# Kernel tuning notes

Hardware: AMD Instinct MI355X
Metric: run time of the kernel (lower is better)

## Reference

```python
import jax, jax.numpy as jnp
import numpy as np

N = 20000      # num_nodes
E = 256000     # num_edges (before self loops)
D_IN = 128
HID = 128      # hidden_dim (per-head out channels)
HEADS = 4
T = 2          # num_timesteps
NEG_SLOPE = 0.2
LN_EPS = 1e-5


def setup_inputs() -> dict:
    key = jax.random.key(0)
    ks = jax.random.split(key, 24)
    def rn(k, shape, s=0.05):
        return jax.random.normal(k, shape, jnp.float32) * s
    HH = HEADS * HID  # 512
    return {
        "x": jax.random.normal(ks[0], (N, D_IN), jnp.float32),
        "edge_index": jax.random.randint(ks[1], (2, E), 0, N),
        # input projection
        "Wp": rn(ks[2], (HID, D_IN)), "bp": jnp.zeros((HID,), jnp.float32),
        # GAT layer 0: in=HID, heads=HEADS, concat
        "W0": rn(ks[3], (HH, HID)), "as0": rn(ks[4], (HEADS, HID)), "ad0": rn(ks[5], (HEADS, HID)), "b0": jnp.zeros((HH,), jnp.float32),
        # GAT layer 1: in=HH, heads=HEADS, concat
        "W1": rn(ks[6], (HH, HH)), "as1": rn(ks[7], (HEADS, HID)), "ad1": rn(ks[8], (HEADS, HID)), "b1": jnp.zeros((HH,), jnp.float32),
        # GAT layer 2 (last): in=HH, heads=1, concat=False
        "W2": rn(ks[9], (HID, HH)), "as2": rn(ks[10], (1, HID)), "ad2": rn(ks[11], (1, HID)), "b2": jnp.zeros((HID,), jnp.float32),
        # layer norms (dims 512, 512, 128)
        "g0": jnp.ones((HH,), jnp.float32), "be0": jnp.zeros((HH,), jnp.float32),
        "g1": jnp.ones((HH,), jnp.float32), "be1": jnp.zeros((HH,), jnp.float32),
        "g2": jnp.ones((HID,), jnp.float32), "be2": jnp.zeros((HID,), jnp.float32),
        # temporal MultiheadAttention (embed=HID, 4 heads)
        "Wqkv": rn(ks[12], (3 * HID, HID)), "bqkv": jnp.zeros((3 * HID,), jnp.float32),
        "Wo": rn(ks[13], (HID, HID)), "bo": jnp.zeros((HID,), jnp.float32),
    }


def _layernorm(x, g, b):
    mu = x.mean(-1, keepdims=True)
    var = ((x - mu) ** 2).mean(-1, keepdims=True)
    return (x - mu) * jax.lax.rsqrt(var + LN_EPS) * g + b


def _gat_conv(h, src, dst, W, a_src, a_dst, bias, heads, concat):
    # h: [N, in]; W: [heads*HID, in]; a_src/a_dst: [heads, HID]
    xp = (h @ W.T).reshape(N, heads, HID)            # [N, heads, HID]
    al_s = (xp * a_src).sum(-1)                      # [N, heads]
    al_d = (xp * a_dst).sum(-1)                      # [N, heads]
    e = jax.nn.leaky_relu(al_s[src] + al_d[dst], NEG_SLOPE)  # [Etot, heads]
    m = jax.ops.segment_max(e, dst, num_segments=N)          # segment softmax over dst
    e = jnp.exp(e - m[dst])
    s = jax.ops.segment_sum(e, dst, num_segments=N)
    alpha = e / (s[dst] + 1e-16)                     # [Etot, heads]
    msg = xp[src] * alpha[:, :, None]                # [Etot, heads, HID]
    out = jax.ops.segment_sum(msg, dst, num_segments=N)      # [N, heads, HID]
    out = out.reshape(N, heads * HID) if concat else out.mean(1)
    return out + bias


def _forward(x, edge_index, Wp, bp, W0, as0, ad0, b0, W1, as1, ad1, b1,
             W2, as2, ad2, b2, g0, be0, g1, be1, g2, be2, Wqkv, bqkv, Wo, bo):
    loops = jnp.arange(N, dtype=edge_index.dtype)    # add_self_loops=True
    src = jnp.concatenate([edge_index[0], loops])
    dst = jnp.concatenate([edge_index[1], loops])

    h = x @ Wp.T + bp                                 # [N, HID]
    layers = [
        (W0, as0, ad0, b0, HEADS, True, g0, be0),
        (W1, as1, ad1, b1, HEADS, True, g1, be1),
        (W2, as2, ad2, b2, 1, False, g2, be2),
    ]
    states = []
    for t in range(T):
        h_t = h
        for i, (W, a_s, a_d, b, heads, concat, g, be) in enumerate(layers):
            h_res = h_t
            h_t = _gat_conv(h_t, src, dst, W, a_s, a_d, b, heads, concat)
            h_t = jax.nn.elu(h_t)
            h_t = _layernorm(h_t, g, be)
            # dropout is identity in eval mode
            if i > 0:
                if h_res.shape[-1] != h_t.shape[-1]:
                    # adaptive_avg_pool1d 512 -> 128: mean over groups of 4
                    r = h_res.shape[-1] // h_t.shape[-1]
                    h_res = h_res.reshape(N, h_t.shape[-1], r).mean(-1)
                h_t = h_t + h_res
        states.append(h_t)
        h = h_t

    ts = jnp.stack(states, axis=1)                    # [N, T, HID]
    # temporal self-attention (4 heads, head_dim = HID//4)
    nh, hd = 4, HID // 4
    qkv = ts @ Wqkv.T + bqkv                          # [N, T, 3*HID]
    q, k, v = jnp.split(qkv, 3, axis=-1)
    q = q.reshape(N, T, nh, hd).transpose(0, 2, 1, 3)
    k = k.reshape(N, T, nh, hd).transpose(0, 2, 1, 3)
    v = v.reshape(N, T, nh, hd).transpose(0, 2, 1, 3)
    attn = jax.nn.softmax(jnp.einsum("nhqd,nhkd->nhqk", q, k) / jnp.sqrt(jnp.float32(hd)), axis=-1)
    o = jnp.einsum("nhqk,nhkd->nhqd", attn, v).transpose(0, 2, 1, 3).reshape(N, T, HID)
    o = o @ Wo.T + bo
    return o.mean(axis=1)                             # [N, HID]


def reference(x, edge_index, Wp, bp, W0, as0, ad0, b0, W1, as1, ad1, b1,
              W2, as2, ad2, b2, g0, be0, g1, be1, g2, be2, Wqkv, bqkv, Wo, bo):
    return _forward(x, edge_index, Wp, bp, W0, as0, ad0, b0, W1, as1, ad1, b1,
                    W2, as2, ad2, b2, g0, be0, g1, be1, g2, be2, Wqkv, bqkv, Wo, bo)
```

## Files before the change

kernel.cpp:

```cpp
#include <hip/hip_runtime.h>
#include <math.h>

#define N_NODES 20000
#define N_EDGES 256000
#define ETOT (N_EDGES + N_NODES)
#define NPAD 20096
#define NPAD2 40064
#define NBLK_SCAN ((N_NODES + 255) / 256)

typedef __attribute__((ext_vector_type(8))) short bf16x8;
typedef __attribute__((ext_vector_type(4))) float f32x4;

__device__ __forceinline__ unsigned short f2bf(float f) {
    unsigned int u = __builtin_bit_cast(unsigned int, f);
    u = (u + 0x7fff + ((u >> 16) & 1)) >> 16;
    return (unsigned short)u;
}

__device__ __forceinline__ float bf2f(unsigned short u) {
    return __builtin_bit_cast(float, (unsigned int)u << 16);
}

__device__ __forceinline__ void gload_lds16(const void* g, void* l) {
    __builtin_amdgcn_global_load_lds(
        (const __attribute__((address_space(1))) void*)g,
        (__attribute__((address_space(3))) void*)l, 16, 0, 0);
}

__device__ __forceinline__ void fma8(float* acc, uint4 v, float w) {
    acc[0] = fmaf(w, __builtin_bit_cast(float, v.x << 16), acc[0]);
    acc[1] = fmaf(w, __builtin_bit_cast(float, v.x & 0xffff0000u), acc[1]);
    acc[2] = fmaf(w, __builtin_bit_cast(float, v.y << 16), acc[2]);
    acc[3] = fmaf(w, __builtin_bit_cast(float, v.y & 0xffff0000u), acc[3]);
    acc[4] = fmaf(w, __builtin_bit_cast(float, v.z << 16), acc[4]);
    acc[5] = fmaf(w, __builtin_bit_cast(float, v.z & 0xffff0000u), acc[5]);
    acc[6] = fmaf(w, __builtin_bit_cast(float, v.w << 16), acc[6]);
    acc[7] = fmaf(w, __builtin_bit_cast(float, v.w & 0xffff0000u), acc[7]);
}


__global__ void hist_kernel(const int* __restrict__ ei, int* __restrict__ cnt) {
    for (int e = blockIdx.x * blockDim.x + threadIdx.x; e < ETOT;
         e += gridDim.x * blockDim.x) {
        int d = (e < N_EDGES) ? ei[N_EDGES + e] : (e - N_EDGES);
        atomicAdd(&cnt[d], 1);
    }
}

__global__ __launch_bounds__(256) void scanA(const int* __restrict__ cnt,
                                             int* __restrict__ incl,
                                             int* __restrict__ bsum) {
    __shared__ int sh[256];
    int t = threadIdx.x;
    int i = blockIdx.x * 256 + t;
    int v = (i < N_NODES) ? cnt[i] : 0;
    sh[t] = v;
    __syncthreads();
#pragma unroll
    for (int off = 1; off < 256; off <<= 1) {
        int u = (t >= off) ? sh[t - off] : 0;
        __syncthreads();
        sh[t] += u;
        __syncthreads();
    }
    if (i < N_NODES) incl[i] = sh[t];
    if (t == 255) bsum[blockIdx.x] = sh[255];
}

__global__ __launch_bounds__(128) void scanB(int* __restrict__ bsum,
                                             int* __restrict__ row_start) {
    __shared__ int sh[128];
    int t = threadIdx.x;
    int v = (t < NBLK_SCAN) ? bsum[t] : 0;
    sh[t] = v;
    __syncthreads();
#pragma unroll
    for (int off = 1; off < 128; off <<= 1) {
        int u = (t >= off) ? sh[t - off] : 0;
        __syncthreads();
        sh[t] += u;
        __syncthreads();
    }
    if (t < NBLK_SCAN) bsum[t] = sh[t] - v;
    if (t == 0) row_start[0] = 0;
}

__global__ __launch_bounds__(256) void scanC(int* __restrict__ cursor,
                                             int* __restrict__ row_start,
                                             const int* __restrict__ bsum) {
    int i = blockIdx.x * 256 + threadIdx.x;
    if (i < N_NODES) {
        int incl = row_start[i + 1] + bsum[blockIdx.x];
        row_start[i + 1] = incl;
        cursor[i] = incl - cursor[i];
    }
}

__global__ void scatter_kernel(const int* __restrict__ ei, int* __restrict__ cursor,
                               int* __restrict__ sorted_id) {
    for (int e = blockIdx.x * blockDim.x + threadIdx.x; e < ETOT;
         e += gridDim.x * blockDim.x) {
        int d = (e < N_EDGES) ? ei[N_EDGES + e] : (e - N_EDGES);
        int pos = atomicAdd(&cursor[d], 1);
        sorted_id[pos] = e;
    }
}

__global__ __launch_bounds__(256) void segsort_kernel(
    const int* __restrict__ ei, const int* __restrict__ row_start,
    int* __restrict__ sorted_id, int* __restrict__ sorted_src) {
    int wv = threadIdx.x >> 6, lane = threadIdx.x & 63;
    int n = blockIdx.x * 4 + wv;
    if (n >= N_NODES) return;
    int base = row_start[n];
    int deg = row_start[n + 1] - base;
    if (deg <= 64) {
        int id = (lane < deg) ? sorted_id[base + lane] : 0x7fffffff;
        int rank = 0;
        for (int j = 0; j < deg; j++) {
            int idj = __shfl(id, j);
            rank += (idj < id);
        }
        if (lane < deg) {
            int src = (id < N_EDGES) ? ei[id] : (id - N_EDGES);
            sorted_src[base + rank] = src;
        }
    } else if (lane == 0) {
        for (int i = base + 1; i < base + deg; i++) {
            int v = sorted_id[i];
            int j = i - 1;
            while (j >= base && sorted_id[j] > v) {
                sorted_id[j + 1] = sorted_id[j];
                j--;
            }
            sorted_id[j + 1] = v;
        }
        for (int i = base; i < base + deg; i++) {
            int id = sorted_id[i];
            sorted_src[i] = (id < N_EDGES) ? ei[id] : (id - N_EDGES);
        }
    }
}

struct SetupArgs {
    const float* s[7];
    unsigned short* d[7];
    int cum[8];
    int* cursor;
    unsigned short* x16;
    unsigned short* h16n;
    unsigned short* h16wA;
    unsigned short* h16wB;
    unsigned short* st16;
    unsigned short* om16;
};

__global__ __launch_bounds__(256) void setup_all(SetupArgs a) {
    int i = blockIdx.x * 256 + threadIdx.x;
    const int PR = NPAD - N_NODES;
    if (i < N_NODES) a.cursor[i] = 0;
    if (i < PR * 128) {
        a.x16[(size_t)N_NODES * 128 + i] = 0;
        a.h16n[(size_t)N_NODES * 128 + i] = 0;
        a.om16[(size_t)N_NODES * 128 + i] = 0;
    }
    if (i < PR * 512) {
        a.h16wA[(size_t)N_NODES * 512 + i] = 0;
        a.h16wB[(size_t)N_NODES * 512 + i] = 0;
    }
    if (i < (NPAD2 - 2 * N_NODES) * 128) a.st16[(size_t)(2 * N_NODES) * 128 + i] = 0;
    if (i < a.cum[7]) {
        int r = 0;
        while (i >= a.cum[r + 1]) r++;
        int off = i - a.cum[r];
        a.d[r][off] = f2bf(a.s[r][off]);
    }
}

__global__ __launch_bounds__(256) void gemm_mfma(
    const unsigned short* __restrict__ A, const unsigned short* __restrict__ B,
    const float* __restrict__ bias, float* __restrict__ Cf,
    unsigned short* __restrict__ C16, int R, int K, int ldc,
    const float* __restrict__ a_s, const float* __restrict__ a_d,
    float* __restrict__ al_s, float* __restrict__ al_d, int H) {
    __shared__ unsigned short Al[64 * 64];
    __shared__ unsigned short Bl[128 * 64];
    __shared__ float red_s[4][32], red_d[4][32];
    int tid = threadIdx.x;
    int lane = tid & 63, wv = tid >> 6;
    int wr = (wv >> 1) * 32, wc = (wv & 1) * 64;
    size_t br = (size_t)blockIdx.x * 64;
    size_t bc = (size_t)blockIdx.y * 128;
    f32x4 acc[2][4] = {};
    for (int k0 = 0; k0 < K; k0 += 64) {
#pragma unroll
        for (int i = 0; i < 2; i++) {
            int idx = i * 256 + tid;
            int row = idx >> 3;
            int kb = (idx & 7) << 4;
            gload_lds16((const char*)(A + (br + row) * K + k0) + kb,
                        (char*)Al + idx * 16);
        }
#pragma unroll
        for (int i = 0; i < 4; i++) {
            int idx = i * 256 + tid;
            int row = idx >> 3;
            int kb = (idx & 7) << 4;
            gload_lds16((const char*)(B + (bc + row) * K + k0) + kb,
                        (char*)Bl + idx * 16);
        }
        __syncthreads();
#pragma unroll
        for (int kk = 0; kk < 2; kk++) {
            bf16x8 af[2], bfr[4];
#pragma unroll
            for (int m = 0; m < 2; m++)
                af[m] = *(const bf16x8*)&Al[(wr + m * 16 + (lane & 15)) * 64 +
                                            kk * 32 + (lane >> 4) * 8];
#pragma unroll
            for (int n = 0; n < 4; n++)
                bfr[n] = *(const bf16x8*)&Bl[(wc + n * 16 + (lane & 15)) * 64 +
                                             kk * 32 + (lane >> 4) * 8];
#pragma unroll
            for (int m = 0; m < 2; m++)
#pragma unroll
                for (int n = 0; n < 4; n++)
                    acc[m][n] = __builtin_amdgcn_mfma_f32_16x16x32_bf16(
                        af[m], bfr[n], acc[m][n], 0, 0, 0);
        }
        __syncthreads();
    }

    if (al_s) {
        float asr[4], adr[4];
#pragma unroll
        for (int n = 0; n < 4; n++) {
            int c = (int)bc + wc + n * 16 + (lane & 15);
            asr[n] = a_s[c];
            adr[n] = a_d[c];
        }
        float ps[2][4], pd[2][4];
#pragma unroll
        for (int m = 0; m < 2; m++)
#pragma unroll
            for (int j = 0; j < 4; j++) {
                float s = 0.f, d = 0.f;
#pragma unroll
                for (int n = 0; n < 4; n++) {
                    float v = acc[m][n][j];
                    s = fmaf(v, asr[n], s);
                    d = fmaf(v, adr[n], d);
                }
#pragma unroll
                for (int off = 8; off; off >>= 1) {
                    s += __shfl_xor(s, off);
                    d += __shfl_xor(d, off);
                }
                ps[m][j] = s;
                pd[m][j] = d;
            }
        if ((lane & 15) == 0) {
#pragma unroll
            for (int m = 0; m < 2; m++)
#pragma unroll
                for (int j = 0; j < 4; j++) {
                    int lr = m * 16 + (lane >> 4) * 4 + j;
                    red_s[wv][lr] = ps[m][j];
                    red_d[wv][lr] = pd[m][j];
                }
        }
        __syncthreads();
        if (tid < 64) {
            int half = tid >> 5, lr = tid & 31;
            float s = red_s[half * 2][lr] + red_s[half * 2 + 1][lr];
            float d = red_d[half * 2][lr] + red_d[half * 2 + 1][lr];
            size_t r = br + half * 32 + lr;
            if (r < (size_t)R) {
                al_s[r * H + blockIdx.y] = s;
                al_d[r * H + blockIdx.y] = d;
            }
        }
    }

#pragma unroll
    for (int m = 0; m < 2; m++) {
        int r0 = wr + m * 16 + (lane >> 4) * 4;
#pragma unroll
        for (int n = 0; n < 4; n++) {
            int c = (int)bc + wc + n * 16 + (lane & 15);
            float bv = bias ? bias[c] : 0.f;
#pragma unroll
            for (int j = 0; j < 4; j++) {
                size_t r = br + r0 + j;
                if (r < (size_t)R) {
                    float v = acc[m][n][j] + bv;
                    if (Cf) Cf[r * ldc + c] = v;
                    if (C16) C16[r * ldc + c] = f2bf(v);
                }
            }
        }
    }
}

template <int RES>
__global__ __launch_bounds__(256) void gat_agg512(
    const unsigned short* __restrict__ xp16, const float* __restrict__ al_s,
    const float* __restrict__ al_d, const int* __restrict__ row_start,
    const int* __restrict__ srcs, const float* __restrict__ bias,
    const float* __restrict__ gamma, const float* __restrict__ beta,
    const unsigned short* __restrict__ h_res16, unsigned short* __restrict__ out16) {
    const int C = 512;
    int tid = threadIdx.x;
    int lane = tid & 63, wv = tid >> 6;
    int n = blockIdx.x * 4 + wv;
    __shared__ int offw[4][64];
    __shared__ float logw[4][256];
    if (n >= N_NODES) return;
    int base = row_start[n];
    int deg = row_start[n + 1] - base;
    int head = lane >> 4;

    float acc[8] = {};
    float scale_end;

    if (deg <= 64) {
        int e_ = lane >> 2, h_ = lane & 3;
        float m = -3.4e38f;
        for (int e0 = 0; e0 < deg; e0 += 16) {
            int e = e0 + e_;
            float v = -3.4e38f;
            if (e < deg) {
                int src = srcs[base + e];
                if (h_ == 0) offw[wv][e] = src * (C * 2);
                float t = al_s[src * 4 + h_] + al_d[n * 4 + h_];
                v = t > 0.f ? t : 0.2f * t;
                logw[wv][e * 4 + h_] = v;
            }
            m = fmaxf(m, v);
        }
#pragma unroll
        for (int off = 4; off <= 32; off <<= 1) m = fmaxf(m, __shfl_xor(m, off));
        float s = 0.f;
        for (int e0 = 0; e0 < deg; e0 += 16) {
            int e = e0 + e_;
            if (e < deg) {
                float p = __expf(logw[wv][e * 4 + h_] - m);
                logw[wv][e * 4 + h_] = p;
                s += p;
            }
        }
#pragma unroll
        for (int off = 4; off <= 32; off <<= 1) s += __shfl_xor(s, off);
        float inv = 1.0f / (s + 1e-16f);
        scale_end = __shfl(inv, head);
        const char* xb = (const char*)xp16 + lane * 16;
#pragma unroll 4
        for (int j = 0; j < deg; j++) {
            float w = logw[wv][j * 4 + head];
            uint4 vv = *(const uint4*)(xb + offw[wv][j]);
            fma8(acc, vv, w);
        }
    } else {
        int e_ = lane >> 2, h_ = lane & 3;
        float m = -3.4e38f;
        for (int e0 = 0; e0 < deg; e0 += 16) {
            int e = e0 + e_;
            if (e < deg) {
                int src = srcs[base + e];
                float t = al_s[src * 4 + h_] + al_d[n * 4 + h_];
                t = t > 0.f ? t : 0.2f * t;
                m = fmaxf(m, t);
            }
        }
#pragma unroll
        for (int off = 4; off <= 32; off <<= 1) m = fmaxf(m, __shfl_xor(m, off));
        float s = 0.f;
        for (int e0 = 0; e0 < deg; e0 += 16) {
            int e = e0 + e_;
            if (e < deg) {
                int src = srcs[base + e];
                float t = al_s[src * 4 + h_] + al_d[n * 4 + h_];
                t = t > 0.f ? t : 0.2f * t;
                s += __expf(t - m);
            }
        }
#pragma unroll
        for (int off = 4; off <= 32; off <<= 1) s += __shfl_xor(s, off);
        float mg = __shfl(m, head);
        float sg = __shfl(s, head);
        float invg = 1.0f / (sg + 1e-16f);
        float aldh = al_d[n * 4 + head];
        const char* xb = (const char*)xp16 + lane * 16;
        for (int j = 0; j < deg; j++) {
            int src = srcs[base + j];
            float t = al_s[src * 4 + head] + aldh;
            t = t > 0.f ? t : 0.2f * t;
            float w = __expf(t - mg) * invg;
            uint4 vv = *(const uint4*)(xb + (size_t)src * (C * 2));
            fma8(acc, vv, w);
        }
        scale_end = 1.0f;
    }

    int ch0 = 8 * lane;
    float vals[8];
    {
        float4 b0 = *(const float4*)&bias[ch0];
        float4 b1 = *(const float4*)&bias[ch0 + 4];
        vals[0] = acc[0] * scale_end + b0.x;
        vals[1] = acc[1] * scale_end + b0.y;
        vals[2] = acc[2] * scale_end + b0.z;
        vals[3] = acc[3] * scale_end + b0.w;
        vals[4] = acc[4] * scale_end + b1.x;
        vals[5] = acc[5] * scale_end + b1.y;
        vals[6] = acc[6] * scale_end + b1.z;
        vals[7] = acc[7] * scale_end + b1.w;
    }
    float s2 = 0.f, q = 0.f;
#pragma unroll
    for (int k = 0; k < 8; k++) {
        vals[k] = vals[k] > 0.f ? vals[k] : (__expf(vals[k]) - 1.0f);
        s2 += vals[k];
        q += vals[k] * vals[k];
    }
#pragma unroll
    for (int off = 1; off <= 32; off <<= 1) {
        s2 += __shfl_xor(s2, off);
        q += __shfl_xor(q, off);
    }
    float mu = s2 / C;
    float var = q / C - mu * mu;
    float rstd = 1.0f / sqrtf(var + 1e-5f);
    {
        float4 g0 = *(const float4*)&gamma[ch0];
        float4 g1 = *(const float4*)&gamma[ch0 + 4];
        float4 be0v = *(const float4*)&beta[ch0];
        float4 be1v = *(const float4*)&beta[ch0 + 4];
        float gg[8] = {g0.x, g0.y, g0.z, g0.w, g1.x, g1.y, g1.z, g1.w};
        float bb[8] = {be0v.x, be0v.y, be0v.z, be0v.w,
                       be1v.x, be1v.y, be1v.z, be1v.w};
#pragma unroll
        for (int k = 0; k < 8; k++) vals[k] = (vals[k] - mu) * rstd * gg[k] + bb[k];
    }
    if (RES == 1) {
        ushort4 r0 = *(const ushort4*)&h_res16[(size_t)n * C + ch0];
        ushort4 r1 = *(const ushort4*)&h_res16[(size_t)n * C + ch0 + 4];
        vals[0] += bf2f(r0.x); vals[1] += bf2f(r0.y);
        vals[2] += bf2f(r0.z); vals[3] += bf2f(r0.w);
        vals[4] += bf2f(r1.x); vals[5] += bf2f(r1.y);
        vals[6] += bf2f(r1.z); vals[7] += bf2f(r1.w);
    }
    uint4 pk;
    pk.x = (unsigned)f2bf(vals[0]) | ((unsigned)f2bf(vals[1]) << 16);
    pk.y = (unsigned)f2bf(vals[2]) | ((unsigned)f2bf(vals[3]) << 16);
    pk.z = (unsigned)f2bf(vals[4]) | ((unsigned)f2bf(vals[5]) << 16);
    pk.w = (unsigned)f2bf(vals[6]) | ((unsigned)f2bf(vals[7]) << 16);
    *(uint4*)&out16[(size_t)n * C + ch0] = pk;
}

__global__ __launch_bounds__(64) void gat_agg128(
    const unsigned short* __restrict__ xp16, const float* __restrict__ al_s,
    const float* __restrict__ al_d, const int* __restrict__ row_start,
    const int* __restrict__ srcs, const float* __restrict__ bias,
    const float* __restrict__ gamma, const float* __restrict__ beta,
    const unsigned short* __restrict__ h_res16, unsigned short* __restrict__ out16,
    unsigned short* __restrict__ out2_16, int out2_stride) {
    const int C = 128;
    int n = blockIdx.x;
    int lane = threadIdx.x & 63;
    __shared__ int off_sh[64];
    __shared__ float w_sh[64];
    __shared__ float m_sh, s_sh;
    int base = row_start[n];
    int deg = row_start[n + 1] - base;

    float acc[8] = {};

    if (deg <= 64) {
        float v = -3.4e38f;
        if (lane < deg) {
            int src = srcs[base + lane];
            off_sh[lane] = src * (C * 2);
            float t = al_s[src] + al_d[n];
            v = t > 0.f ? t : 0.2f * t;
        }
        float m = v;
#pragma unroll
        for (int off = 32; off; off >>= 1) m = fmaxf(m, __shfl_xor(m, off));
        float p = (lane < deg) ? __expf(v - m) : 0.f;
        float s = p;
#pragma unroll
        for (int off = 32; off; off >>= 1) s += __shfl_xor(s, off);
        s += 1e-16f;
        if (lane < deg) w_sh[lane] = p / s;
        __syncthreads();
        int li = lane & 15, rg = lane >> 4;
        const char* xb = (const char*)xp16 + li * 16;
        for (int j = rg; j < deg; j += 4) {
            uint4 vv = *(const uint4*)(xb + off_sh[j]);
            fma8(acc, vv, w_sh[j]);
        }
    } else {
        float ald = al_d[n];
        float m = -3.4e38f;
        for (int e = lane; e < deg; e += 64) {
            float v = al_s[srcs[base + e]] + ald;
            v = v > 0.f ? v : 0.2f * v;
            m = fmaxf(m, v);
        }
#pragma unroll
        for (int off = 32; off; off >>= 1) m = fmaxf(m, __shfl_xor(m, off));
        float s = 0.f;
        for (int e = lane; e < deg; e += 64) {
            float v = al_s[srcs[base + e]] + ald;
            v = v > 0.f ? v : 0.2f * v;
            s += __expf(v - m);
        }
#pragma unroll
        for (int off = 32; off; off >>= 1) s += __shfl_xor(s, off);
        if (lane == 0) { m_sh = m; s_sh = s + 1e-16f; }
        __syncthreads();
        float mh = m_sh, ssh = s_sh;
        int li = lane & 15, rg = lane >> 4;
        const char* xb = (const char*)xp16 + li * 16;
        for (int j = rg; j < deg; j += 4) {
            int src = srcs[base + j];
            float t = al_s[src] + ald;
            t = t > 0.f ? t : 0.2f * t;
            float w = __expf(t - mh) / ssh;
            uint4 vv = *(const uint4*)(xb + (size_t)src * (C * 2));
            fma8(acc, vv, w);
        }
    }

#pragma unroll
    for (int k = 0; k < 8; k++) {
        acc[k] += __shfl_xor(acc[k], 16);
        acc[k] += __shfl_xor(acc[k], 32);
    }
    int li = lane & 15;
    int ch0 = 8 * li;
    float vals[8];
    float4 b0 = *(const float4*)&bias[ch0];
    float4 b1 = *(const float4*)&bias[ch0 + 4];
    vals[0] = acc[0] + b0.x; vals[1] = acc[1] + b0.y;
    vals[2] = acc[2] + b0.z; vals[3] = acc[3] + b0.w;
    vals[4] = acc[4] + b1.x; vals[5] = acc[5] + b1.y;
    vals[6] = acc[6] + b1.z; vals[7] = acc[7] + b1.w;
    float s = 0.f, q = 0.f;
#pragma unroll
    for (int k = 0; k < 8; k++) {
        vals[k] = vals[k] > 0.f ? vals[k] : (__expf(vals[k]) - 1.0f);
        s += vals[k];
        q += vals[k] * vals[k];
    }
#pragma unroll
    for (int off = 8; off; off >>= 1) {
        s += __shfl_xor(s, off);
        q += __shfl_xor(q, off);
    }
    float mu = s / C;
    float var = q / C - mu * mu;
    float rstd = 1.0f / sqrtf(var + 1e-5f);
    float4 g0 = *(const float4*)&gamma[ch0];
    float4 g1 = *(const float4*)&gamma[ch0 + 4];
    float4 be0v = *(const float4*)&beta[ch0];
    float4 be1v = *(const float4*)&beta[ch0 + 4];
    float gg[8] = {g0.x, g0.y, g0.z, g0.w, g1.x, g1.y, g1.z, g1.w};
    float bb[8] = {be0v.x, be0v.y, be0v.z, be0v.w, be1v.x, be1v.y, be1v.z, be1v.w};
#pragma unroll
    for (int k = 0; k < 8; k++) vals[k] = (vals[k] - mu) * rstd * gg[k] + bb[k];
    {
        const unsigned short* r = &h_res16[(size_t)n * 512 + 4 * ch0];
#pragma unroll
        for (int k = 0; k < 8; k++) {
            ushort4 rv = *(const ushort4*)&r[4 * k];
            vals[k] += 0.25f * (bf2f(rv.x) + bf2f(rv.y) + bf2f(rv.z) + bf2f(rv.w));
        }
    }
    if (lane < 16) {
        uint4 pk;
        pk.x = (unsigned)f2bf(vals[0]) | ((unsigned)f2bf(vals[1]) << 16);
        pk.y = (unsigned)f2bf(vals[2]) | ((unsigned)f2bf(vals[3]) << 16);
        pk.z = (unsigned)f2bf(vals[4]) | ((unsigned)f2bf(vals[5]) << 16);
        pk.w = (unsigned)f2bf(vals[6]) | ((unsigned)f2bf(vals[7]) << 16);
        if (out16) *(uint4*)&out16[(size_t)n * C + ch0] = pk;
        if (out2_16) *(uint4*)&out2_16[(size_t)n * out2_stride + ch0] = pk;
    }
}

__global__ __launch_bounds__(128) void temporal_attn(
    const unsigned short* __restrict__ qkv16, unsigned short* __restrict__ om16) {
    __shared__ float sh[768];
    int n = blockIdx.x;
    int c = threadIdx.x;
    for (int i = c; i < 768; i += 128) {
        int t = i / 384;
        sh[i] = bf2f(qkv16[(size_t)(n * 2 + t) * 384 + (i - t * 384)]);
    }
    __syncthreads();
    int head = c >> 5;
    int hb = head * 32;
    const float scale = 0.17677669529663687f;
    float o[2];
#pragma unroll
    for (int qt = 0; qt < 2; qt++) {
        float s0 = 0.f, s1 = 0.f;
#pragma unroll
        for (int d = 0; d < 32; d++) {
            float qv = sh[qt * 384 + hb + d];
            s0 = fmaf(qv, sh[0 * 384 + 128 + hb + d], s0);
            s1 = fmaf(qv, sh[1 * 384 + 128 + hb + d], s1);
        }
        s0 *= scale; s1 *= scale;
        float m = fmaxf(s0, s1);
        float p0 = __expf(s0 - m), p1 = __expf(s1 - m);
        float inv = 1.0f / (p0 + p1);
        o[qt] = p0 * inv * sh[0 * 384 + 256 + c] + p1 * inv * sh[1 * 384 + 256 + c];
    }
    om16[(size_t)n * 128 + c] = f2bf(0.5f * (o[0] + o[1]));
}


extern "C" void kernel_launch(void* const* d_in, const int* in_sizes, int n_in,
                              void* d_out, int out_size, void* d_ws, size_t ws_size,
                              hipStream_t stream) {
    const float* x   = (const float*)d_in[0];
    const int*   ei  = (const int*)d_in[1];
    const float* Wp  = (const float*)d_in[2];
    const float* bp  = (const float*)d_in[3];
    const float* W0  = (const float*)d_in[4];
    const float* as0 = (const float*)d_in[5];
    const float* ad0 = (const float*)d_in[6];
    const float* b0  = (const float*)d_in[7];
    const float* W1  = (const float*)d_in[8];
    const float* as1 = (const float*)d_in[9];
    const float* ad1 = (const float*)d_in[10];
    const float* b1  = (const float*)d_in[11];
    const float* W2  = (const float*)d_in[12];
    const float* as2 = (const float*)d_in[13];
    const float* ad2 = (const float*)d_in[14];
    const float* b2  = (const float*)d_in[15];
    const float* g0  = (const float*)d_in[16];
    const float* be0 = (const float*)d_in[17];
    const float* g1  = (const float*)d_in[18];
    const float* be1 = (const float*)d_in[19];
    const float* g2  = (const float*)d_in[20];
    const float* be2 = (const float*)d_in[21];
    const float* Wqkv = (const float*)d_in[22];
    const float* bqkv = (const float*)d_in[23];
    const float* Wo  = (const float*)d_in[24];
    const float* bo  = (const float*)d_in[25];
    float* out = (float*)d_out;

    const int N = N_NODES;
    float* f = (float*)d_ws;
    float* als = f;
    float* ald = als + (size_t)N * 4;
    int* row_start  = (int*)(ald + (size_t)N * 4);
    int* cursor     = row_start + (N + 1);
    int* sorted_id  = cursor + N;
    int* sorted_src = sorted_id + ETOT;
    int* bsum       = sorted_src + ETOT;
    uintptr_t pa = (uintptr_t)(bsum + NBLK_SCAN + 1);
    pa = (pa + 63) & ~(uintptr_t)63;
    unsigned short* x16   = (unsigned short*)pa;
    unsigned short* h16n  = x16 + (size_t)NPAD * 128;
    unsigned short* h16wA = h16n + (size_t)NPAD * 128;
    unsigned short* h16wB = h16wA + (size_t)NPAD * 512;
    unsigned short* xp16  = h16wB + (size_t)NPAD * 512;
    unsigned short* st16  = xp16 + (size_t)NPAD * 512;
    unsigned short* qkv16 = st16 + (size_t)NPAD2 * 128;
    unsigned short* om16  = qkv16 + (size_t)NPAD2 * 384;
    unsigned short* w16   = om16 + (size_t)NPAD * 128;
    unsigned short* Wp16   = w16;
    unsigned short* W016   = Wp16 + 128 * 128;
    unsigned short* W116   = W016 + 512 * 128;
    unsigned short* W216   = W116 + 512 * 512;
    unsigned short* Wqkv16 = W216 + 128 * 512;
    unsigned short* Wo16   = Wqkv16 + 384 * 128;

    {
        SetupArgs a;
        const float* srcs7[7] = {Wp, W0, W1, W2, Wqkv, Wo, x};
        unsigned short* dsts7[7] = {Wp16, W016, W116, W216, Wqkv16, Wo16, x16};
        int sizes7[7] = {128 * 128, 512 * 128, 512 * 512, 128 * 512,
                         384 * 128, 128 * 128, N_NODES * 128};
        int c = 0;
        a.cum[0] = 0;
        for (int i = 0; i < 7; i++) {
            a.s[i] = srcs7[i];
            a.d[i] = dsts7[i];
            c += sizes7[i];
            a.cum[i + 1] = c;
        }
        a.cursor = cursor;
        a.x16 = x16; a.h16n = h16n; a.h16wA = h16wA; a.h16wB = h16wB;
        a.st16 = st16; a.om16 = om16;
        setup_all<<<(c + 255) / 256, 256, 0, stream>>>(a);
    }

    hist_kernel<<<1024, 256, 0, stream>>>(ei, cursor);
    scanA<<<NBLK_SCAN, 256, 0, stream>>>(cursor, row_start + 1, bsum);
    scanB<<<1, 128, 0, stream>>>(bsum, row_start);
    scanC<<<NBLK_SCAN, 256, 0, stream>>>(cursor, row_start, bsum);
    scatter_kernel<<<1024, 256, 0, stream>>>(ei, cursor, sorted_id);
    segsort_kernel<<<(N + 3) / 4, 256, 0, stream>>>(ei, row_start, sorted_id,
                                                    sorted_src);

    const int GX = NPAD / 64;
    const int GX2 = NPAD2 / 64;
    const int GA = (N + 3) / 4;
    {
        dim3 g(GX, 1);
        gemm_mfma<<<g, 256, 0, stream>>>(x16, Wp16, bp, nullptr, h16n, N, 128, 128,
                                         nullptr, nullptr, nullptr, nullptr, 0);
    }

    for (int t = 0; t < 2; t++) {
        {
            dim3 g(GX, 4);
            gemm_mfma<<<g, 256, 0, stream>>>(h16n, W016, nullptr, nullptr, xp16,
                                             N, 128, 512, as0, ad0, als, ald, 4);
            gat_agg512<0><<<GA, 256, 0, stream>>>(
                xp16, als, ald, row_start, sorted_src, b0, g0, be0, nullptr, h16wA);
        }
        {
            dim3 g(GX, 4);
            gemm_mfma<<<g, 256, 0, stream>>>(h16wA, W116, nullptr, nullptr, xp16,
                                             N, 512, 512, as1, ad1, als, ald, 4);
            gat_agg512<1><<<GA, 256, 0, stream>>>(
                xp16, als, ald, row_start, sorted_src, b1, g1, be1, h16wA, h16wB);
        }
        {
            dim3 g(GX, 1);
            gemm_mfma<<<g, 256, 0, stream>>>(h16wB, W216, nullptr, nullptr, xp16,
                                             N, 512, 128, as2, ad2, als, ald, 1);
            gat_agg128<<<N, 64, 0, stream>>>(
                xp16, als, ald, row_start, sorted_src, b2, g2, be2, h16wB,
                (t == 0) ? h16n : nullptr, st16 + (size_t)t * 128, 256);
        }
    }

    {
        dim3 g(GX2, 3);
        gemm_mfma<<<g, 256, 0, stream>>>(st16, Wqkv16, bqkv, nullptr, qkv16,
                                         2 * N, 128, 384, nullptr, nullptr,
                                         nullptr, nullptr, 0);
    }
    temporal_attn<<<N, 128, 0, stream>>>(qkv16, om16);
    {
        dim3 g(GX, 1);
        gemm_mfma<<<g, 256, 0, stream>>>(om16, Wo16, bo, out, nullptr,
                                         N, 128, 128, nullptr, nullptr,
                                         nullptr, nullptr, 0);
    }
}
```

Before: 475.0 us.

## Process two destination nodes per wavefront in 512-wide GAT aggregation

Each wavefront in gat_agg512 now handles two consecutive destination nodes instead of one. When both have degree at most 64, their neighbor gathers are interleaved in one loop so that two independent memory loads are in flight per iteration, aiming to hide gather latency. Shared-memory staging doubles and the grid halves. The trade-offs are more registers per thread (two accumulators), fewer wavefronts overall, and uneven work when the two degrees differ.

New measurement: 552.3 us. 16.3% more time.

```diff
diff --git a/kernel.cpp b/kernel.cpp
--- a/kernel.cpp
+++ b/kernel.cpp
@@ -312,150 +312,185 @@
     const int C = 512;
     int tid = threadIdx.x;
     int lane = tid & 63, wv = tid >> 6;
-    int n = blockIdx.x * 4 + wv;
-    __shared__ int offw[4][64];
-    __shared__ float logw[4][256];
-    if (n >= N_NODES) return;
-    int base = row_start[n];
-    int deg = row_start[n + 1] - base;
+    int n0 = blockIdx.x * 8 + 2 * wv;
+    __shared__ int offw[4][128];
+    __shared__ float logw[4][512];
+    if (n0 >= N_NODES) return;
+    bool two = (n0 + 1 < N_NODES);
     int head = lane >> 4;
-
-    float acc[8] = {};
-    float scale_end;
-
-    if (deg <= 64) {
-        int e_ = lane >> 2, h_ = lane & 3;
-        float m = -3.4e38f;
-        for (int e0 = 0; e0 < deg; e0 += 16) {
-            int e = e0 + e_;
-            float v = -3.4e38f;
-            if (e < deg) {
-                int src = srcs[base + e];
-                if (h_ == 0) offw[wv][e] = src * (C * 2);
-                float t = al_s[src * 4 + h_] + al_d[n * 4 + h_];
-                v = t > 0.f ? t : 0.2f * t;
-                logw[wv][e * 4 + h_] = v;
-            }
-            m = fmaxf(m, v);
-        }
-#pragma unroll
-        for (int off = 4; off <= 32; off <<= 1) m = fmaxf(m, __shfl_xor(m, off));
-        float s = 0.f;
-        for (int e0 = 0; e0 < deg; e0 += 16) {
-            int e = e0 + e_;
-            if (e < deg) {
-                float p = __expf(logw[wv][e * 4 + h_] - m);
-                logw[wv][e * 4 + h_] = p;
-                s += p;
-            }
-        }
-#pragma unroll
-        for (int off = 4; off <= 32; off <<= 1) s += __shfl_xor(s, off);
-        float inv = 1.0f / (s + 1e-16f);
-        scale_end = __shfl(inv, head);
-        const char* xb = (const char*)xp16 + lane * 16;
+    int e_ = lane >> 2, h_ = lane & 3;
+
+    int baseA[2], degA[2];
+    baseA[0] = row_start[n0];
+    degA[0] = row_start[n0 + 1] - baseA[0];
+    baseA[1] = 0; degA[1] = 0;
+    if (two) {
+        baseA[1] = row_start[n0 + 1];
+        degA[1] = row_start[n0 + 2] - baseA[1];
+    }
+
+    float acc[2][8] = {};
+    float scaleA[2] = {1.f, 1.f};
+    bool fastA[2];
+    fastA[0] = (degA[0] <= 64);
+    fastA[1] = (degA[1] <= 64);
+
+    for (int nn = 0; nn < 2; nn++) {
+        if (nn == 1 && !two) break;
+        int n = n0 + nn, base = baseA[nn], deg = degA[nn];
+        if (fastA[nn]) {
+            float m = -3.4e38f;
+            for (int e0 = 0; e0 < deg; e0 += 16) {
+                int e = e0 + e_;
+                float v = -3.4e38f;
+                if (e < deg) {
+                    int src = srcs[base + e];
+                    if (h_ == 0) offw[wv][nn * 64 + e] = src * (C * 2);
+                    float t = al_s[src * 4 + h_] + al_d[n * 4 + h_];
+                    v = t > 0.f ? t : 0.2f * t;
+                    logw[wv][nn * 256 + e * 4 + h_] = v;
+                }
+                m = fmaxf(m, v);
+            }
+#pragma unroll
+            for (int off = 4; off <= 32; off <<= 1)
+                m = fmaxf(m, __shfl_xor(m, off));
+            float s = 0.f;
+            for (int e0 = 0; e0 < deg; e0 += 16) {
+                int e = e0 + e_;
+                if (e < deg) {
+                    float p = __expf(logw[wv][nn * 256 + e * 4 + h_] - m);
+                    logw[wv][nn * 256 + e * 4 + h_] = p;
+                    s += p;
+                }
+            }
+#pragma unroll
+            for (int off = 4; off <= 32; off <<= 1) s += __shfl_xor(s, off);
+            float inv = 1.0f / (s + 1e-16f);
+            scaleA[nn] = __shfl(inv, head);
+        }
+    }
+
+    const char* xb = (const char*)xp16 + lane * 16;
+    if (fastA[0] && fastA[1] && two) {
+        int dmax = max(degA[0], degA[1]);
+#pragma unroll 2
+        for (int j = 0; j < dmax; j++) {
+            if (j < degA[0]) {
+                float w = logw[wv][j * 4 + head];
+                uint4 vv = *(const uint4*)(xb + offw[wv][j]);
+                fma8(acc[0], vv, w);
+            }
+            if (j < degA[1]) {
+                float w = logw[wv][256 + j * 4 + head];
+                uint4 vv = *(const uint4*)(xb + offw[wv][64 + j]);
+                fma8(acc[1], vv, w);
+            }
+        }
+    } else {
+        for (int nn = 0; nn < 2; nn++) {
+            if (nn == 1 && !two) break;
+            int n = n0 + nn, base = baseA[nn], deg = degA[nn];
+            if (fastA[nn]) {
 #pragma unroll 4
-        for (int j = 0; j < deg; j++) {
-            float w = logw[wv][j * 4 + head];
-            uint4 vv = *(const uint4*)(xb + offw[wv][j]);
-            fma8(acc, vv, w);
-        }
-    } else {
-        int e_ = lane >> 2, h_ = lane & 3;
-        float m = -3.4e38f;
-        for (int e0 = 0; e0 < deg; e0 += 16) {
-            int e = e0 + e_;
-            if (e < deg) {
-                int src = srcs[base + e];
-                float t = al_s[src * 4 + h_] + al_d[n * 4 + h_];
-                t = t > 0.f ? t : 0.2f * t;
-                m = fmaxf(m, t);
-            }
-        }
-#pragma unroll
-        for (int off = 4; off <= 32; off <<= 1) m = fmaxf(m, __shfl_xor(m, off));
-        float s = 0.f;
-        for (int e0 = 0; e0 < deg; e0 += 16) {
-            int e = e0 + e_;
-            if (e < deg) {
-                int src = srcs[base + e];
-                float t = al_s[src * 4 + h_] + al_d[n * 4 + h_];
-                t = t > 0.f ? t : 0.2f * t;
-                s += __expf(t - m);
-            }
-        }
-#pragma unroll
-        for (int off = 4; off <= 32; off <<= 1) s += __shfl_xor(s, off);
-        float mg = __shfl(m, head);
-        float sg = __shfl(s, head);
-        float invg = 1.0f / (sg + 1e-16f);
-        float aldh = al_d[n * 4 + head];
-        const char* xb = (const char*)xp16 + lane * 16;
-        for (int j = 0; j < deg; j++) {
-            int src = srcs[base + j];
-            float t = al_s[src * 4 + head] + aldh;
-            t = t > 0.f ? t : 0.2f * t;
-            float w = __expf(t - mg) * invg;
-            uint4 vv = *(const uint4*)(xb + (size_t)src * (C * 2));
-            fma8(acc, vv, w);
-        }
-        scale_end = 1.0f;
+                for (int j = 0; j < deg; j++) {
+                    float w = logw[wv][nn * 256 + j * 4 + head];
+                    uint4 vv = *(const uint4*)(xb + offw[wv][nn * 64 + j]);
+                    fma8(acc[nn], vv, w);
+                }
+            } else {
+                float m = -3.4e38f;
+                for (int e0 = 0; e0 < deg; e0 += 16) {
+                    int e = e0 + e_;
+                    if (e < deg) {
+                        int src = srcs[base + e];
+                        float t = al_s[src * 4 + h_] + al_d[n * 4 + h_];
+                        t = t > 0.f ? t : 0.2f * t;
+                        m = fmaxf(m, t);
+                    }
+                }
+#pragma unroll
+                for (int off = 4; off <= 32; off <<= 1)
+                    m = fmaxf(m, __shfl_xor(m, off));
+                float s = 0.f;
+                for (int e0 = 0; e0 < deg; e0 += 16) {
+                    int e = e0 + e_;
+                    if (e < deg) {
+                        int src = srcs[base + e];
+                        float t = al_s[src * 4 + h_] + al_d[n * 4 + h_];
+                        t = t > 0.f ? t : 0.2f * t;
+                        s += __expf(t - m);
+                    }
+                }
+#pragma unroll
+                for (int off = 4; off <= 32; off <<= 1) s += __shfl_xor(s, off);
+                float mg = __shfl(m, head);
+                float sg = __shfl(s, head);
+                float invg = 1.0f / (sg + 1e-16f);
+                float aldh = al_d[n * 4 + head];
+                for (int j = 0; j < deg; j++) {
+                    int src = srcs[base + j];
+                    float t = al_s[src * 4 + head] + aldh;
+                    t = t > 0.f ? t : 0.2f * t;
+                    float w = __expf(t - mg) * invg;
+                    uint4 vv = *(const uint4*)(xb + (size_t)src * (C * 2));
+                    fma8(acc[nn], vv, w);
+                }
+                scaleA[nn] = 1.0f;
+            }
+        }
     }
 
     int ch0 = 8 * lane;
-    float vals[8];
-    {
-        float4 b0 = *(const float4*)&bias[ch0];
-        float4 b1 = *(const float4*)&bias[ch0 + 4];
-        vals[0] = acc[0] * scale_end + b0.x;
-        vals[1] = acc[1] * scale_end + b0.y;
-        vals[2] = acc[2] * scale_end + b0.z;
-        vals[3] = acc[3] * scale_end + b0.w;
-        vals[4] = acc[4] * scale_end + b1.x;
-        vals[5] = acc[5] * scale_end + b1.y;
-        vals[6] = acc[6] * scale_end + b1.z;
-        vals[7] = acc[7] * scale_end + b1.w;
-    }
-    float s2 = 0.f, q = 0.f;
-#pragma unroll
-    for (int k = 0; k < 8; k++) {
-        vals[k] = vals[k] > 0.f ? vals[k] : (__expf(vals[k]) - 1.0f);
-        s2 += vals[k];
-        q += vals[k] * vals[k];
-    }
-#pragma unroll
-    for (int off = 1; off <= 32; off <<= 1) {
-        s2 += __shfl_xor(s2, off);
-        q += __shfl_xor(q, off);
-    }
-    float mu = s2 / C;
-    float var = q / C - mu * mu;
-    float rstd = 1.0f / sqrtf(var + 1e-5f);
-    {
-        float4 g0 = *(const float4*)&gamma[ch0];
-        float4 g1 = *(const float4*)&gamma[ch0 + 4];
-        float4 be0v = *(const float4*)&beta[ch0];
-        float4 be1v = *(const float4*)&beta[ch0 + 4];
-        float gg[8] = {g0.x, g0.y, g0.z, g0.w, g1.x, g1.y, g1.z, g1.w};
-        float bb[8] = {be0v.x, be0v.y, be0v.z, be0v.w,
-                       be1v.x, be1v.y, be1v.z, be1v.w};
+    float4 b0 = *(const float4*)&bias[ch0];
+    float4 b1 = *(const float4*)&bias[ch0 + 4];
+    float4 g0 = *(const float4*)&gamma[ch0];
+    float4 g1 = *(const float4*)&gamma[ch0 + 4];
+    float4 be0v = *(const float4*)&beta[ch0];
+    float4 be1v = *(const float4*)&beta[ch0 + 4];
+    float bbia[8] = {b0.x, b0.y, b0.z, b0.w, b1.x, b1.y, b1.z, b1.w};
+    float gg[8] = {g0.x, g0.y, g0.z, g0.w, g1.x, g1.y, g1.z, g1.w};
+    float bb[8] = {be0v.x, be0v.y, be0v.z, be0v.w, be1v.x, be1v.y, be1v.z, be1v.w};
+
+    for (int nn = 0; nn < 2; nn++) {
+        if (nn == 1 && !two) break;
+        int n = n0 + nn;
+        float se = scaleA[nn];
+        float vals[8];
+        float s2 = 0.f, q = 0.f;
+#pragma unroll
+        for (int k = 0; k < 8; k++) {
+            float v = acc[nn][k] * se + bbia[k];
+            v = v > 0.f ? v : (__expf(v) - 1.0f);
+            vals[k] = v;
+            s2 += v;
+            q += v * v;
+        }
+#pragma unroll
+        for (int off = 1; off <= 32; off <<= 1) {
+            s2 += __shfl_xor(s2, off);
+            q += __shfl_xor(q, off);
+        }
+        float mu = s2 / C;
+        float var = q / C - mu * mu;
+        float rstd = 1.0f / sqrtf(var + 1e-5f);
 #pragma unroll
         for (int k = 0; k < 8; k++) vals[k] = (vals[k] - mu) * rstd * gg[k] + bb[k];
-    }
-    if (RES == 1) {
-        ushort4 r0 = *(const ushort4*)&h_res16[(size_t)n * C + ch0];
-        ushort4 r1 = *(const ushort4*)&h_res16[(size_t)n * C + ch0 + 4];
-        vals[0] += bf2f(r0.x); vals[1] += bf2f(r0.y);
-        vals[2] += bf2f(r0.z); vals[3] += bf2f(r0.w);
-        vals[4] += bf2f(r1.x); vals[5] += bf2f(r1.y);
-        vals[6] += bf2f(r1.z); vals[7] += bf2f(r1.w);
-    }
-    uint4 pk;
-    pk.x = (unsigned)f2bf(vals[0]) | ((unsigned)f2bf(vals[1]) << 16);
-    pk.y = (unsigned)f2bf(vals[2]) | ((unsigned)f2bf(vals[3]) << 16);
-    pk.z = (unsigned)f2bf(vals[4]) | ((unsigned)f2bf(vals[5]) << 16);
-    pk.w = (unsigned)f2bf(vals[6]) | ((unsigned)f2bf(vals[7]) << 16);
-    *(uint4*)&out16[(size_t)n * C + ch0] = pk;
+        if (RES == 1) {
+            ushort4 r0 = *(const ushort4*)&h_res16[(size_t)n * C + ch0];
+            ushort4 r1 = *(const ushort4*)&h_res16[(size_t)n * C + ch0 + 4];
+            vals[0] += bf2f(r0.x); vals[1] += bf2f(r0.y);
+            vals[2] += bf2f(r0.z); vals[3] += bf2f(r0.w);
+            vals[4] += bf2f(r1.x); vals[5] += bf2f(r1.y);
+            vals[6] += bf2f(r1.z); vals[7] += bf2f(r1.w);
+        }
+        uint4 pk;
+        pk.x = (unsigned)f2bf(vals[0]) | ((unsigned)f2bf(vals[1]) << 16);
+        pk.y = (unsigned)f2bf(vals[2]) | ((unsigned)f2bf(vals[3]) << 16);
+        pk.z = (unsigned)f2bf(vals[4]) | ((unsigned)f2bf(vals[5]) << 16);
+        pk.w = (unsigned)f2bf(vals[6]) | ((unsigned)f2bf(vals[7]) << 16);
+        *(uint4*)&out16[(size_t)n * C + ch0] = pk;
+    }
 }
 
 __global__ __launch_bounds__(64) void gat_agg128(
@@ -710,7 +745,7 @@
 
     const int GX = NPAD / 64;
     const int GX2 = NPAD2 / 64;
-    const int GA = (N + 3) / 4;
+    const int GA = (N + 7) / 8;
     {
         dim3 g(GX, 1);
         gemm_mfma<<<g, 256, 0, stream>>>(x16, Wp16, bp, nullptr, h16n, N, 128, 128,
```

## Reorder GAT layer 0 to aggregate 128-dim inputs before per-head projection

Applied to the files above, without the earlier changes.

For the first GAT layer, attention logits are now computed directly from the 128-dim input using precomputed W0^T·a vectors (ahat). Neighbor aggregation is done on the narrow 128-wide features per head, and the per-head projection is applied afterward through a block-diagonal GEMM mode (lda/adiag). Bias, ELU and layernorm then run in a separate ln512 kernel. This is meant to cut the gather traffic of the edge aggregation from 512-wide projected rows to 128-wide rows, at the cost of extra launches and an extra bf16 intermediate pass.

After: 474.8 us. Within noise of the previous version (-0.0%).

```diff
diff --git a/kernel.cpp b/kernel.cpp
--- a/kernel.cpp
+++ b/kernel.cpp
@@ -151,6 +151,7 @@
     unsigned short* h16n;
     unsigned short* h16wA;
     unsigned short* h16wB;
+    unsigned short* xp16;
     unsigned short* st16;
     unsigned short* om16;
 };
@@ -167,6 +168,7 @@
     if (i < PR * 512) {
         a.h16wA[(size_t)N_NODES * 512 + i] = 0;
         a.h16wB[(size_t)N_NODES * 512 + i] = 0;
+        a.xp16[(size_t)N_NODES * 512 + i] = 0;
     }
     if (i < (NPAD2 - 2 * N_NODES) * 128) a.st16[(size_t)(2 * N_NODES) * 128 + i] = 0;
     if (i < a.cum[7]) {
@@ -177,12 +179,62 @@
     }
 }
 
+__global__ __launch_bounds__(512) void make_ahat(
+    const unsigned short* __restrict__ W016, const float* __restrict__ as0,
+    const float* __restrict__ ad0, float* __restrict__ ahat_s,
+    float* __restrict__ ahat_d) {
+    int t = threadIdx.x;
+    int h = t >> 7, k = t & 127;
+    float ss = 0.f, sd = 0.f;
+    for (int c = 0; c < 128; c++) {
+        float w = bf2f(W016[(size_t)(h * 128 + c) * 128 + k]);
+        ss = fmaf(as0[h * 128 + c], w, ss);
+        sd = fmaf(ad0[h * 128 + c], w, sd);
+    }
+    ahat_s[t] = ss;
+    ahat_d[t] = sd;
+}
+
+__global__ __launch_bounds__(256) void coef128(
+    const unsigned short* __restrict__ h16n, const float* __restrict__ ahat_s,
+    const float* __restrict__ ahat_d, float* __restrict__ als,
+    float* __restrict__ ald) {
+    int wv = threadIdx.x >> 6, lane = threadIdx.x & 63;
+    int n = blockIdx.x * 4 + wv;
+    if (n >= N_NODES) return;
+    int k0 = 2 * lane;
+    float h0 = bf2f(h16n[(size_t)n * 128 + k0]);
+    float h1 = bf2f(h16n[(size_t)n * 128 + k0 + 1]);
+    float accs[4], accd[4];
+#pragma unroll
+    for (int h = 0; h < 4; h++) {
+        accs[h] = h0 * ahat_s[h * 128 + k0] + h1 * ahat_s[h * 128 + k0 + 1];
+        accd[h] = h0 * ahat_d[h * 128 + k0] + h1 * ahat_d[h * 128 + k0 + 1];
+    }
+#pragma unroll
+    for (int off = 1; off <= 32; off <<= 1) {
+#pragma unroll
+        for (int h = 0; h < 4; h++) {
+            accs[h] += __shfl_xor(accs[h], off);
+            accd[h] += __shfl_xor(accd[h], off);
+        }
+    }
+    if (lane == 0) {
+#pragma unroll
+        for (int h = 0; h < 4; h++) {
+            als[n * 4 + h] = accs[h];
+            ald[n * 4 + h] = accd[h];
+        }
+    }
+}
+
 __global__ __launch_bounds__(256) void gemm_mfma(
     const unsigned short* __restrict__ A, const unsigned short* __restrict__ B,
     const float* __restrict__ bias, float* __restrict__ Cf,
     unsigned short* __restrict__ C16, int R, int K, int ldc,
     const float* __restrict__ a_s, const float* __restrict__ a_d,
-    float* __restrict__ al_s, float* __restrict__ al_d, int H) {
+    float* __restrict__ al_s, float* __restrict__ al_d, int H,
+    int lda, int adiag) {
     __shared__ unsigned short Al[64 * 64];
     __shared__ unsigned short Bl[128 * 64];
     __shared__ float red_s[4][32], red_d[4][32];
@@ -191,6 +243,7 @@
     int wr = (wv >> 1) * 32, wc = (wv & 1) * 64;
     size_t br = (size_t)blockIdx.x * 64;
     size_t bc = (size_t)blockIdx.y * 128;
+    int acol = adiag ? (int)blockIdx.y * K : 0;
     f32x4 acc[2][4] = {};
     for (int k0 = 0; k0 < K; k0 += 64) {
 #pragma unroll
@@ -198,7 +251,7 @@
             int idx = i * 256 + tid;
             int row = idx >> 3;
             int kb = (idx & 7) << 4;
-            gload_lds16((const char*)(A + (br + row) * K + k0) + kb,
+            gload_lds16((const char*)(A + (br + row) * lda + acol + k0) + kb,
                         (char*)Al + idx * 16);
         }
 #pragma unroll
@@ -450,6 +503,163 @@
         vals[4] += bf2f(r1.x); vals[5] += bf2f(r1.y);
         vals[6] += bf2f(r1.z); vals[7] += bf2f(r1.w);
     }
+    uint4 pk;
+    pk.x = (unsigned)f2bf(vals[0]) | ((unsigned)f2bf(vals[1]) << 16);
+    pk.y = (unsigned)f2bf(vals[2]) | ((unsigned)f2bf(vals[3]) << 16);
+    pk.z = (unsigned)f2bf(vals[4]) | ((unsigned)f2bf(vals[5]) << 16);
+    pk.w = (unsigned)f2bf(vals[6]) | ((unsigned)f2bf(vals[7]) << 16);
+    *(uint4*)&out16[(size_t)n * C + ch0] = pk;
+}
+
+__global__ __launch_bounds__(256) void gat_gather128(
+    const unsigned short* __restrict__ h16n, const float* __restrict__ al_s,
+    const float* __restrict__ al_d, const int* __restrict__ row_start,
+    const int* __restrict__ srcs, unsigned short* __restrict__ s16) {
+    int tid = threadIdx.x;
+    int lane = tid & 63, wv = tid >> 6;
+    int n = blockIdx.x * 4 + wv;
+    __shared__ int offw[4][64];
+    __shared__ float logw[4][256];
+    if (n >= N_NODES) return;
+    int base = row_start[n];
+    int deg = row_start[n + 1] - base;
+    int head = lane >> 4;
+    int li = lane & 15;
+
+    float acc[8] = {};
+    float scale_end;
+
+    if (deg <= 64) {
+        int e_ = lane >> 2, h_ = lane & 3;
+        float m = -3.4e38f;
+        for (int e0 = 0; e0 < deg; e0 += 16) {
+            int e = e0 + e_;
+            float v = -3.4e38f;
+            if (e < deg) {
+                int src = srcs[base + e];
+                if (h_ == 0) offw[wv][e] = src * 256;
+                float t = al_s[src * 4 + h_] + al_d[n * 4 + h_];
+                v = t > 0.f ? t : 0.2f * t;
+                logw[wv][e * 4 + h_] = v;
+            }
+            m = fmaxf(m, v);
+        }
+#pragma unroll
+        for (int off = 4; off <= 32; off <<= 1) m = fmaxf(m, __shfl_xor(m, off));
+        float s = 0.f;
+        for (int e0 = 0; e0 < deg; e0 += 16) {
+            int e = e0 + e_;
+            if (e < deg) {
+                float p = __expf(logw[wv][e * 4 + h_] - m);
+                logw[wv][e * 4 + h_] = p;
+                s += p;
+            }
+        }
+#pragma unroll
+        for (int off = 4; off <= 32; off <<= 1) s += __shfl_xor(s, off);
+        float inv = 1.0f / (s + 1e-16f);
+        scale_end = __shfl(inv, head);
+        const char* xb = (const char*)h16n + li * 16;
+#pragma unroll 4
+        for (int j = 0; j < deg; j++) {
+            float w = logw[wv][j * 4 + head];
+            uint4 vv = *(const uint4*)(xb + offw[wv][j]);
+            fma8(acc, vv, w);
+        }
+    } else {
+        int e_ = lane >> 2, h_ = lane & 3;
+        float m = -3.4e38f;
+        for (int e0 = 0; e0 < deg; e0 += 16) {
+            int e = e0 + e_;
+            if (e < deg) {
+                int src = srcs[base + e];
+                float t = al_s[src * 4 + h_] + al_d[n * 4 + h_];
+                t = t > 0.f ? t : 0.2f * t;
+                m = fmaxf(m, t);
+            }
+        }
+#pragma unroll
+        for (int off = 4; off <= 32; off <<= 1) m = fmaxf(m, __shfl_xor(m, off));
+        float s = 0.f;
+        for (int e0 = 0; e0 < deg; e0 += 16) {
+            int e = e0 + e_;
+            if (e < deg) {
+                int src = srcs[base + e];
+                float t = al_s[src * 4 + h_] + al_d[n * 4 + h_];
+                t = t > 0.f ? t : 0.2f * t;
+                s += __expf(t - m);
+            }
+        }
+#pragma unroll
+        for (int off = 4; off <= 32; off <<= 1) s += __shfl_xor(s, off);
+        float mg = __shfl(m, head);
+        float sg = __shfl(s, head);
+        float invg = 1.0f / (sg + 1e-16f);
+        float aldh = al_d[n * 4 + head];
+        const char* xb = (const char*)h16n + li * 16;
+        for (int j = 0; j < deg; j++) {
+            int src = srcs[base + j];
+            float t = al_s[src * 4 + head] + aldh;
+            t = t > 0.f ? t : 0.2f * t;
+            float w = __expf(t - mg) * invg;
+            uint4 vv = *(const uint4*)(xb + (size_t)src * 256);
+            fma8(acc, vv, w);
+        }
+        scale_end = 1.0f;
+    }
+
+    uint4 pk;
+    pk.x = (unsigned)f2bf(acc[0] * scale_end) | ((unsigned)f2bf(acc[1] * scale_end) << 16);
+    pk.y = (unsigned)f2bf(acc[2] * scale_end) | ((unsigned)f2bf(acc[3] * scale_end) << 16);
+    pk.z = (unsigned)f2bf(acc[4] * scale_end) | ((unsigned)f2bf(acc[5] * scale_end) << 16);
+    pk.w = (unsigned)f2bf(acc[6] * scale_end) | ((unsigned)f2bf(acc[7] * scale_end) << 16);
+    *(uint4*)&s16[(size_t)n * 512 + 8 * lane] = pk;
+}
+
+__global__ __launch_bounds__(256) void ln512(
+    const unsigned short* __restrict__ proj16, const float* __restrict__ bias,
+    const float* __restrict__ gamma, const float* __restrict__ beta,
+    unsigned short* __restrict__ out16) {
+    const int C = 512;
+    int lane = threadIdx.x & 63, wv = threadIdx.x >> 6;
+    int n = blockIdx.x * 4 + wv;
+    if (n >= N_NODES) return;
+    int ch0 = 8 * lane;
+    uint4 pv = *(const uint4*)&proj16[(size_t)n * C + ch0];
+    float4 b0 = *(const float4*)&bias[ch0];
+    float4 b1 = *(const float4*)&bias[ch0 + 4];
+    float vals[8];
+    vals[0] = __builtin_bit_cast(float, pv.x << 16) + b0.x;
+    vals[1] = __builtin_bit_cast(float, pv.x & 0xffff0000u) + b0.y;
+    vals[2] = __builtin_bit_cast(float, pv.y << 16) + b0.z;
+    vals[3] = __builtin_bit_cast(float, pv.y & 0xffff0000u) + b0.w;
+    vals[4] = __builtin_bit_cast(float, pv.z << 16) + b1.x;
+    vals[5] = __builtin_bit_cast(float, pv.z & 0xffff0000u) + b1.y;
+    vals[6] = __builtin_bit_cast(float, pv.w << 16) + b1.z;
+    vals[7] = __builtin_bit_cast(float, pv.w & 0xffff0000u) + b1.w;
+    float s2 = 0.f, q = 0.f;
+#pragma unroll
+    for (int k = 0; k < 8; k++) {
+        vals[k] = vals[k] > 0.f ? vals[k] : (__expf(vals[k]) - 1.0f);
+        s2 += vals[k];
+        q += vals[k] * vals[k];
+    }
+#pragma unroll
+    for (int off = 1; off <= 32; off <<= 1) {
+        s2 += __shfl_xor(s2, off);
+        q += __shfl_xor(q, off);
+    }
+    float mu = s2 / C;
+    float var = q / C - mu * mu;
+    float rstd = 1.0f / sqrtf(var + 1e-5f);
+    float4 g0 = *(const float4*)&gamma[ch0];
+    float4 g1 = *(const float4*)&gamma[ch0 + 4];
+    float4 be0v = *(const float4*)&beta[ch0];
+    float4 be1v = *(const float4*)&beta[ch0 + 4];
+    float gg[8] = {g0.x, g0.y, g0.z, g0.w, g1.x, g1.y, g1.z, g1.w};
+    float bb[8] = {be0v.x, be0v.y, be0v.z, be0v.w, be1v.x, be1v.y, be1v.z, be1v.w};
+#pragma unroll
+    for (int k = 0; k < 8; k++) vals[k] = (vals[k] - mu) * rstd * gg[k] + bb[k];
     uint4 pk;
     pk.x = (unsigned)f2bf(vals[0]) | ((unsigned)f2bf(vals[1]) << 16);
     pk.y = (unsigned)f2bf(vals[2]) | ((unsigned)f2bf(vals[3]) << 16);
@@ -657,7 +867,9 @@
     float* f = (float*)d_ws;
     float* als = f;
     float* ald = als + (size_t)N * 4;
-    int* row_start  = (int*)(ald + (size_t)N * 4);
+    float* ahat_s = ald + (size_t)N * 4;
+    float* ahat_d = ahat_s + 512;
+    int* row_start  = (int*)(ahat_d + 512);
     int* cursor     = row_start + (N + 1);
     int* sorted_id  = cursor + N;
     int* sorted_src = sorted_id + ETOT;
@@ -696,9 +908,10 @@
         }
         a.cursor = cursor;
         a.x16 = x16; a.h16n = h16n; a.h16wA = h16wA; a.h16wB = h16wB;
-        a.st16 = st16; a.om16 = om16;
+        a.xp16 = xp16; a.st16 = st16; a.om16 = om16;
         setup_all<<<(c + 255) / 256, 256, 0, stream>>>(a);
     }
+    make_ahat<<<1, 512, 0, stream>>>(W016, as0, ad0, ahat_s, ahat_d);
 
     hist_kernel<<<1024, 256, 0, stream>>>(ei, cursor);
     scanA<<<NBLK_SCAN, 256, 0, stream>>>(cursor, row_start + 1, bsum);
@@ -714,28 +927,34 @@
     {
         dim3 g(GX, 1);
         gemm_mfma<<<g, 256, 0, stream>>>(x16, Wp16, bp, nullptr, h16n, N, 128, 128,
-                                         nullptr, nullptr, nullptr, nullptr, 0);
+                                         nullptr, nullptr, nullptr, nullptr, 0,
+                                         128, 0);
     }
 
     for (int t = 0; t < 2; t++) {
         {
+            coef128<<<GA, 256, 0, stream>>>(h16n, ahat_s, ahat_d, als, ald);
+            gat_gather128<<<GA, 256, 0, stream>>>(h16n, als, ald, row_start,
+                                                  sorted_src, xp16);
             dim3 g(GX, 4);
-            gemm_mfma<<<g, 256, 0, stream>>>(h16n, W016, nullptr, nullptr, xp16,
-                                             N, 128, 512, as0, ad0, als, ald, 4);
-            gat_agg512<0><<<GA, 256, 0, stream>>>(
-                xp16, als, ald, row_start, sorted_src, b0, g0, be0, nullptr, h16wA);
+            gemm_mfma<<<g, 256, 0, stream>>>(xp16, W016, nullptr, nullptr, h16wB,
+                                             N, 128, 512, nullptr, nullptr,
+                                             nullptr, nullptr, 0, 512, 1);
+            ln512<<<GA, 256, 0, stream>>>(h16wB, b0, g0, be0, h16wA);
         }
         {
             dim3 g(GX, 4);
             gemm_mfma<<<g, 256, 0, stream>>>(h16wA, W116, nullptr, nullptr, xp16,
-                                             N, 512, 512, as1, ad1, als, ald, 4);
+                                             N, 512, 512, as1, ad1, als, ald, 4,
+                                             512, 0);
             gat_agg512<1><<<GA, 256, 0, stream>>>(
                 xp16, als, ald, row_start, sorted_src, b1, g1, be1, h16wA, h16wB);
         }
         {
             dim3 g(GX, 1);
             gemm_mfma<<<g, 256, 0, stream>>>(h16wB, W216, nullptr, nullptr, xp16,
-                                             N, 512, 128, as2, ad2, als, ald, 1);
+                                             N, 512, 128, as2, ad2, als, ald, 1,
+                                             512, 0);
             gat_agg128<<<N, 64, 0, stream>>>(
                 xp16, als, ald, row_start, sorted_src, b2, g2, be2, h16wB,
                 (t == 0) ? h16n : nullptr, st16 + (size_t)t * 128, 256);
@@ -746,13 +965,13 @@
         dim3 g(GX2, 3);
         gemm_mfma<<<g, 256, 0, stream>>>(st16, Wqkv16, bqkv, nullptr, qkv16,
                                          2 * N, 128, 384, nullptr, nullptr,
-                                         nullptr, nullptr, 0);
+                                         nullptr, nullptr, 0, 128, 0);
     }
     temporal_attn<<<N, 128, 0, stream>>>(qkv16, om16);
     {
         dim3 g(GX, 1);
         gemm_mfma<<<g, 256, 0, stream>>>(om16, Wo16, bo, out, nullptr,
                                          N, 128, 128, nullptr, nullptr,
-                                         nullptr, nullptr, 0);
-    }
-}
+                                         nullptr, nullptr, 0, 128, 0);
+    }
+}
```
